# Performance work log

Hardware: AMD Instinct MI355X
Metric: run time of the kernel (lower is better)

## Reference

```python
import jax, jax.numpy as jnp
import numpy as np

IMG = 144      # image height/width
P = 4          # patch size
NP = IMG // P  # patches per side (36)
N = NP * NP * (IMG // NP // P if False else 1) * (IMG * IMG // (P * P) // (NP * NP))  # placeholder
N = IMG * IMG // (P * P)  # 1296 tokens (C=1)
E = P * P      # embedding dim = 16


def setup_inputs() -> dict:
    key = jax.random.key(0)
    x = jax.random.uniform(key, (4, 1, IMG, IMG), dtype=jnp.float32)
    return {"x": x}


def reference(x) -> jnp.ndarray:
    B = x.shape[0]
    x_max = jnp.max(x)
    xn = x / x_max

    # SimplePatching: img.unfold(3,P,P).unfold(4,P,P).reshape(B,-1,P*P)
    # For C=1 this flattening is exactly row-major reshape: each token is a
    # 1xP^2 horizontal strip of pixels.
    tkn = xn.reshape(B, N, E)  # (B, N, E)

    # SimpleMSA with n_heads=1 (forced by the repeat/view), scale=1.0:
    # attn[b,i,j] = softmax_j( -mean_d (t_i - t_j)^2 )
    diff = tkn[:, :, None, :] - tkn[:, None, :, :]        # (B, N, N, E)
    d2 = jnp.mean(jnp.square(diff), axis=-1)              # (B, N, N)
    attn = jax.nn.softmax(-d2, axis=-1)                   # (B, N, N)
    out = jnp.einsum('bij,bjd->bid', attn, tkn)           # (B, N, E)

    # SimpleMerging: view(B,1,N,P^2) -> permute -> view(B,P^2,N) -> F.fold
    # fold with kernel=stride=P is a pure permutation reshape:
    # out_img[b, by*P+ky, bx*P+kx] = m[b, ky*P+kx, by*NP+bx]
    m = out.transpose(0, 2, 1)                            # (B, P^2, N)
    m = m.reshape(B, P, P, NP, NP)                        # (B, ky, kx, by, bx)
    img = m.transpose(0, 3, 1, 4, 2).reshape(B, 1, IMG, IMG)
    return img * x_max
```

## Files before the change

### kernel.cpp

```cpp
#include <hip/hip_runtime.h>
#include <hip/hip_bf16.h>

#define IMGX   144
#define PATCH  4
#define NPS    36
#define NTOKB  1296
#define ED     16
#define BATCH  4
#define NTOK   5184
#define CH     64
#define LSTRIDE 20
#define PREP_BLOCKS 21

__device__ float g_partial[PREP_BLOCKS];
__device__ float g_norms[NTOK];

__global__ __launch_bounds__(256) void prep_kernel(const float* __restrict__ x) {
    __shared__ float wmax[4];
    const int tid = threadIdx.x;
    const int t = blockIdx.x * 256 + tid;
    float m = 0.0f;
    if (t < NTOK) {
        const float4* p = (const float4*)(x + t * ED);
        float v[16];
        float4* v4 = (float4*)v;
        v4[0] = p[0];
        v4[1] = p[1];
        v4[2] = p[2];
        v4[3] = p[3];
        float ns = 0.0f;
#pragma unroll
        for (int k = 0; k < 16; k++) {
            ns = fmaf(v[k], v[k], ns);
            m = fmaxf(m, v[k]);
        }
        g_norms[t] = ns;
    }
#pragma unroll
    for (int s = 32; s; s >>= 1) m = fmaxf(m, __shfl_xor(m, s));
    if ((tid & 63) == 0) wmax[tid >> 6] = m;
    __syncthreads();
    if (tid == 0) {
        float bm = fmaxf(fmaxf(wmax[0], wmax[1]), fmaxf(wmax[2], wmax[3]));
        g_partial[blockIdx.x] = bm;
    }
}

__global__ __launch_bounds__(256) void attn_kernel(const float* __restrict__ x,
                                                   float* __restrict__ out) {
    __shared__ float lds[CH * LSTRIDE];

    const int tid  = threadIdx.x;
    const int lane = tid & 63;
    const int wave = tid >> 6;
    const int blk  = blockIdx.x;
    const int b    = blk / 324;
    const int i    = (blk % 324) * 4 + wave;

    const float* xb = x + b * (NTOKB * ED);
    const float* norms = g_norms + b * NTOKB;

    float pm = (lane < PREP_BLOCKS) ? g_partial[lane] : 0.0f;
#pragma unroll
    for (int sh = 32; sh; sh >>= 1) pm = fmaxf(pm, __shfl_xor(pm, sh));
    const float xmax = pm;
    const float s = 1.0f / (16.0f * xmax * xmax);

    float ti[16];
    {
        const float4* p = (const float4*)(xb + i * ED);
        float4* t4 = (float4*)ti;
        t4[0] = p[0];
        t4[1] = p[1];
        t4[2] = p[2];
        t4[3] = p[3];
    }
    const float m = s * norms[i];

    float o[16];
#pragma unroll
    for (int d = 0; d < 16; d++) o[d] = 0.0f;
    float denom = 0.0f;

    const int tok = tid >> 2;
    const int q   = tid & 3;

    for (int j0 = 0; j0 < NTOKB; j0 += CH) {
        __syncthreads();
        {
            int j = j0 + tok;
            if (j < NTOKB) {
                const float4 v = *((const float4*)(xb + j * ED + q * 4));
                *((float4*)&lds[tok * LSTRIDE + q * 4]) = v;
            }
        }
        __syncthreads();

        const int jj = j0 + lane;
        if (jj < NTOKB) {
            float tj[16];
            float4* tj4 = (float4*)tj;
            const float4* lp = (const float4*)&lds[lane * LSTRIDE];
            tj4[0] = lp[0];
            tj4[1] = lp[1];
            tj4[2] = lp[2];
            tj4[3] = lp[3];

            const float nj = norms[jj];
            float dot = 0.0f;
#pragma unroll
            for (int d = 0; d < 16; d++) dot = fmaf(ti[d], tj[d], dot);

            const float pj = __expf(fmaf(s, fmaf(2.0f, dot, -nj), -m));
            denom += pj;
#pragma unroll
            for (int d = 0; d < 16; d++) o[d] = fmaf(pj, tj[d], o[d]);
        }
    }

#pragma unroll
    for (int sh = 32; sh; sh >>= 1) {
        denom += __shfl_xor(denom, sh);
#pragma unroll
        for (int d = 0; d < 16; d++) o[d] += __shfl_xor(o[d], sh);
    }

    const float inv = 1.0f / denom;

    if (lane < 4) {
        const int by = i / NPS;
        const int bx = i % NPS;
        const int ky = lane;
        float4 sv;
        sv.x = o[ky * 4 + 0] * inv;
        sv.y = o[ky * 4 + 1] * inv;
        sv.z = o[ky * 4 + 2] * inv;
        sv.w = o[ky * 4 + 3] * inv;
        float* dst = out + b * (IMGX * IMGX) + (by * PATCH + ky) * IMGX + bx * PATCH;
        *((float4*)dst) = sv;
    }
}

extern "C" void kernel_launch(void* const* d_in, const int* in_sizes, int n_in,
                              void* d_out, int out_size, void* d_ws, size_t ws_size,
                              hipStream_t stream) {
    const float* x = (const float*)d_in[0];
    float* out = (float*)d_out;
    (void)d_ws; (void)ws_size;

    hipLaunchKernelGGL(prep_kernel, dim3(PREP_BLOCKS), dim3(256), 0, stream, x);
    hipLaunchKernelGGL(attn_kernel, dim3(1296), dim3(256), 0, stream, x, out);
}
```

Baseline: 73.89 us.

## Process four query rows per single-wave block with double-buffered key tiles

Measured after the change: 103.2 us. +39.7%, slower.

```diff
diff --git a/kernel.cpp b/kernel.cpp
--- a/kernel.cpp
+++ b/kernel.cpp
@@ -1,5 +1,4 @@
 #include <hip/hip_runtime.h>
-#include <hip/hip_bf16.h>
 
 #define IMGX   144
 #define PATCH  4
@@ -9,7 +8,10 @@
 #define BATCH  4
 #define NTOK   5184
 #define CH     64
-#define LSTRIDE 20
+#define NCHUNK 21
+#define LSTR   20
+#define RPW    4
+#define BPB    324
 #define PREP_BLOCKS 21
 
 __device__ float g_partial[PREP_BLOCKS];
@@ -24,10 +26,7 @@
         const float4* p = (const float4*)(x + t * ED);
         float v[16];
         float4* v4 = (float4*)v;
-        v4[0] = p[0];
-        v4[1] = p[1];
-        v4[2] = p[2];
-        v4[3] = p[3];
+        v4[0] = p[0]; v4[1] = p[1]; v4[2] = p[2]; v4[3] = p[3];
         float ns = 0.0f;
 #pragma unroll
         for (int k = 0; k < 16; k++) {
@@ -41,104 +40,158 @@
     if ((tid & 63) == 0) wmax[tid >> 6] = m;
     __syncthreads();
     if (tid == 0) {
-        float bm = fmaxf(fmaxf(wmax[0], wmax[1]), fmaxf(wmax[2], wmax[3]));
-        g_partial[blockIdx.x] = bm;
+        g_partial[blockIdx.x] = fmaxf(fmaxf(wmax[0], wmax[1]), fmaxf(wmax[2], wmax[3]));
     }
 }
 
-__global__ __launch_bounds__(256) void attn_kernel(const float* __restrict__ x,
-                                                   float* __restrict__ out) {
-    __shared__ float lds[CH * LSTRIDE];
-
-    const int tid  = threadIdx.x;
-    const int lane = tid & 63;
-    const int wave = tid >> 6;
-    const int blk  = blockIdx.x;
-    const int b    = blk / 324;
-    const int i    = (blk % 324) * 4 + wave;
-
-    const float* xb = x + b * (NTOKB * ED);
-    const float* norms = g_norms + b * NTOKB;
+__global__ __launch_bounds__(64) void attn_kernel(const float* __restrict__ x,
+                                                  float* __restrict__ out) {
+    __shared__ float lds[2][CH * LSTR];
+
+    const int lane = threadIdx.x;
+    const int wid  = blockIdx.x;
+    const int b    = wid / BPB;
+    const int i0   = (wid - b * BPB) * RPW;
+
+    const float* __restrict__ xb    = x + b * (NTOKB * ED);
+    const float* __restrict__ norms = g_norms + b * NTOKB;
 
     float pm = (lane < PREP_BLOCKS) ? g_partial[lane] : 0.0f;
 #pragma unroll
     for (int sh = 32; sh; sh >>= 1) pm = fmaxf(pm, __shfl_xor(pm, sh));
     const float xmax = pm;
-    const float s = 1.0f / (16.0f * xmax * xmax);
-
-    float ti[16];
+    const float s  = 1.0f / (16.0f * xmax * xmax);
+    const float c2 = 2.0f * s * 1.4426950408889634f;
+    const float cn = s * 1.4426950408889634f;
+
+    float ti[RPW][16];
+#pragma unroll
+    for (int r = 0; r < RPW; r++) {
+        const float4* p = (const float4*)(xb + (i0 + r) * ED);
+#pragma unroll
+        for (int q = 0; q < 4; q++) {
+            const float4 a = p[q];
+            ti[r][q * 4 + 0] = a.x * c2;
+            ti[r][q * 4 + 1] = a.y * c2;
+            ti[r][q * 4 + 2] = a.z * c2;
+            ti[r][q * 4 + 3] = a.w * c2;
+        }
+    }
+
+    float o[RPW][16];
+#pragma unroll
+    for (int r = 0; r < RPW; r++)
+#pragma unroll
+        for (int k = 0; k < 16; k++) o[r][k] = 0.0f;
+    float den0 = 0.0f, den1 = 0.0f, den2 = 0.0f, den3 = 0.0f;
+
+    const int stok = lane >> 2;
+    const int sq   = lane & 3;
+
+    float4 st[4];
+    float njnext;
     {
-        const float4* p = (const float4*)(xb + i * ED);
-        float4* t4 = (float4*)ti;
-        t4[0] = p[0];
-        t4[1] = p[1];
-        t4[2] = p[2];
-        t4[3] = p[3];
-    }
-    const float m = s * norms[i];
-
-    float o[16];
-#pragma unroll
-    for (int d = 0; d < 16; d++) o[d] = 0.0f;
-    float denom = 0.0f;
-
-    const int tok = tid >> 2;
-    const int q   = tid & 3;
-
-    for (int j0 = 0; j0 < NTOKB; j0 += CH) {
-        __syncthreads();
-        {
-            int j = j0 + tok;
-            if (j < NTOKB) {
-                const float4 v = *((const float4*)(xb + j * ED + q * 4));
-                *((float4*)&lds[tok * LSTRIDE + q * 4]) = v;
-            }
-        }
+#pragma unroll
+        for (int q = 0; q < 4; q++)
+            st[q] = ((const float4*)(xb + (q * 16 + stok) * ED))[sq];
+        njnext = norms[lane];
+    }
+#pragma unroll
+    for (int q = 0; q < 4; q++)
+        *((float4*)&lds[0][(q * 16 + stok) * LSTR + sq * 4]) = st[q];
+
+    for (int c = 0; c < NCHUNK; c++) {
+        const int j0 = c * CH;
+        const float njcur = njnext;
+
+        if (c + 1 < NCHUNK) {
+            const int jb = j0 + CH;
+#pragma unroll
+            for (int q = 0; q < 4; q++) {
+                const int jt = jb + q * 16 + stok;
+                float4 z; z.x = z.y = z.z = z.w = 0.0f;
+                st[q] = (jt < NTOKB) ? ((const float4*)(xb + jt * ED))[sq] : z;
+            }
+            const int jn = jb + lane;
+            njnext = (jn < NTOKB) ? norms[jn] : 0.0f;
+        }
+
         __syncthreads();
 
         const int jj = j0 + lane;
         if (jj < NTOKB) {
             float tj[16];
-            float4* tj4 = (float4*)tj;
-            const float4* lp = (const float4*)&lds[lane * LSTRIDE];
-            tj4[0] = lp[0];
-            tj4[1] = lp[1];
-            tj4[2] = lp[2];
-            tj4[3] = lp[3];
-
-            const float nj = norms[jj];
-            float dot = 0.0f;
-#pragma unroll
-            for (int d = 0; d < 16; d++) dot = fmaf(ti[d], tj[d], dot);
-
-            const float pj = __expf(fmaf(s, fmaf(2.0f, dot, -nj), -m));
-            denom += pj;
-#pragma unroll
-            for (int d = 0; d < 16; d++) o[d] = fmaf(pj, tj[d], o[d]);
+            {
+                const float4* lp = (const float4*)&lds[c & 1][lane * LSTR];
+                ((float4*)tj)[0] = lp[0];
+                ((float4*)tj)[1] = lp[1];
+                ((float4*)tj)[2] = lp[2];
+                ((float4*)tj)[3] = lp[3];
+            }
+            float d0 = 0.0f, d1 = 0.0f, d2 = 0.0f, d3 = 0.0f;
+#pragma unroll
+            for (int k = 0; k < 16; k++) {
+                const float t = tj[k];
+                d0 = fmaf(ti[0][k], t, d0);
+                d1 = fmaf(ti[1][k], t, d1);
+                d2 = fmaf(ti[2][k], t, d2);
+                d3 = fmaf(ti[3][k], t, d3);
+            }
+            const float cc = cn * njcur;
+            const float e0 = exp2f(d0 - cc);
+            const float e1 = exp2f(d1 - cc);
+            const float e2 = exp2f(d2 - cc);
+            const float e3 = exp2f(d3 - cc);
+            den0 += e0; den1 += e1; den2 += e2; den3 += e3;
+#pragma unroll
+            for (int k = 0; k < 16; k++) {
+                const float t = tj[k];
+                o[0][k] = fmaf(e0, t, o[0][k]);
+                o[1][k] = fmaf(e1, t, o[1][k]);
+                o[2][k] = fmaf(e2, t, o[2][k]);
+                o[3][k] = fmaf(e3, t, o[3][k]);
+            }
+        }
+
+        if (c + 1 < NCHUNK) {
+#pragma unroll
+            for (int q = 0; q < 4; q++)
+                *((float4*)&lds[(c + 1) & 1][(q * 16 + stok) * LSTR + sq * 4]) = st[q];
         }
     }
 
 #pragma unroll
     for (int sh = 32; sh; sh >>= 1) {
-        denom += __shfl_xor(denom, sh);
-#pragma unroll
-        for (int d = 0; d < 16; d++) o[d] += __shfl_xor(o[d], sh);
-    }
-
-    const float inv = 1.0f / denom;
-
-    if (lane < 4) {
-        const int by = i / NPS;
-        const int bx = i % NPS;
-        const int ky = lane;
-        float4 sv;
-        sv.x = o[ky * 4 + 0] * inv;
-        sv.y = o[ky * 4 + 1] * inv;
-        sv.z = o[ky * 4 + 2] * inv;
-        sv.w = o[ky * 4 + 3] * inv;
-        float* dst = out + b * (IMGX * IMGX) + (by * PATCH + ky) * IMGX + bx * PATCH;
-        *((float4*)dst) = sv;
-    }
+        den0 += __shfl_xor(den0, sh);
+        den1 += __shfl_xor(den1, sh);
+        den2 += __shfl_xor(den2, sh);
+        den3 += __shfl_xor(den3, sh);
+    }
+
+#define V(n) o[(n) >> 4][(n) & 15]
+#pragma unroll
+    for (int m = 32; m; m >>= 1) {
+        const bool hi = (lane & m) != 0;
+#pragma unroll
+        for (int k = 0; k < m; k++) {
+            const float give = hi ? V(k) : V(k + m);
+            const float got  = __shfl_xor(give, m);
+            V(k) = (hi ? V(k + m) : V(k)) + got;
+        }
+    }
+
+    const float dl = (lane & 16) ? den1 : den0;
+    const float dh = (lane & 16) ? den3 : den2;
+    const float dd = (lane & 32) ? dh : dl;
+    const float val = V(0) / dd;
+
+    const int r  = lane >> 4;
+    const int d  = lane & 15;
+    const int i  = i0 + r;
+    const int by = i / NPS;
+    const int bx = i - by * NPS;
+    out[b * (IMGX * IMGX) + (by * PATCH + (d >> 2)) * IMGX + bx * PATCH + (d & 3)] = val;
+#undef V
 }
 
 extern "C" void kernel_launch(void* const* d_in, const int* in_sizes, int n_in,
@@ -149,5 +202,5 @@
     (void)d_ws; (void)ws_size;
 
     hipLaunchKernelGGL(prep_kernel, dim3(PREP_BLOCKS), dim3(256), 0, stream, x);
-    hipLaunchKernelGGL(attn_kernel, dim3(1296), dim3(256), 0, stream, x, out);
+    hipLaunchKernelGGL(attn_kernel, dim3(NTOKB), dim3(64), 0, stream, x, out);
 }
```
